# Kernel optimization log

Measured on AMD Instinct MI355X. Metric: run time of the kernel, lower is better.

Reference implementation:

```python
import jax, jax.numpy as jnp
import numpy as np

N_EMBED = 384
NUM_HEADS = 6
HEAD_SIZE = 64
B, T = 128, 256


def setup_inputs() -> dict:
    key = jax.random.key(0)
    ks = jax.random.split(key, 6)
    x = jax.random.normal(ks[0], (B, T, N_EMBED), dtype=jnp.float32)
    s = 0.02
    Wq = jax.random.normal(ks[1], (NUM_HEADS, N_EMBED, HEAD_SIZE), dtype=jnp.float32) * s
    Wk = jax.random.normal(ks[2], (NUM_HEADS, N_EMBED, HEAD_SIZE), dtype=jnp.float32) * s
    Wv = jax.random.normal(ks[3], (NUM_HEADS, N_EMBED, HEAD_SIZE), dtype=jnp.float32) * s
    Wp = jax.random.normal(ks[4], (NUM_HEADS * HEAD_SIZE, N_EMBED), dtype=jnp.float32) * s
    bp = jnp.zeros((N_EMBED,), dtype=jnp.float32)
    return {"x": x, "Wq": Wq, "Wk": Wk, "Wv": Wv, "Wp": Wp, "bp": bp}


def reference(x, Wq, Wk, Wv, Wp, bp):
    # x: [B,T,C]; Wq/Wk/Wv: [H,C,hs]; Wp: [H*hs, C]
    Bx, Tx, C = x.shape
    q = jnp.einsum('btc,hcd->bhtd', x, Wq)
    k = jnp.einsum('btc,hcd->bhtd', x, Wk)
    v = jnp.einsum('btc,hcd->bhtd', x, Wv)
    scale = HEAD_SIZE ** (-0.5)
    scores = jnp.einsum('bhtd,bhsd->bhts', q, k) * scale  # [B,H,T,T]
    causal = jnp.tril(jnp.ones((Tx, Tx), dtype=bool))
    scores = jnp.where(causal, scores, -jnp.inf)
    attn = jax.nn.softmax(scores, axis=-1)
    # dropout is identity in eval mode
    out = jnp.einsum('bhts,bhsd->bhtd', attn, v)  # [B,H,T,hs]
    out = out.transpose(0, 2, 1, 3).reshape(Bx, Tx, NUM_HEADS * HEAD_SIZE)
    return out @ Wp + bp
```

## Files before the change

### kernel.cpp

```cpp
#include <hip/hip_runtime.h>
#include <hip/hip_bf16.h>

#define C_DIM 384
#define H_NUM 6
#define HS    64
#define B_DIM 128
#define T_DIM 256
#define NROWS (B_DIM * T_DIM)

typedef unsigned short u16;
typedef unsigned int u32;
typedef short bf16x8 __attribute__((ext_vector_type(8)));
typedef float floatx4 __attribute__((ext_vector_type(4)));

__device__ __forceinline__ u16 f2b(float f) {
  __hip_bfloat16 h = __float2bfloat16(f);
  u16 u;
  __builtin_memcpy(&u, &h, 2);
  return u;
}
__device__ __forceinline__ void gload_lds16(const void* g, void* lds) {
  __builtin_amdgcn_global_load_lds(
      (const __attribute__((address_space(1))) u32*)g,
      (__attribute__((address_space(3))) u32*)lds, 16, 0, 0);
}

__global__ __launch_bounds__(256) void prep_kernel(
    const float* __restrict__ x, const float* __restrict__ Wq,
    const float* __restrict__ Wk, const float* __restrict__ Wv,
    const float* __restrict__ Wp, u16* __restrict__ xb,
    u16* __restrict__ Wh, u16* __restrict__ Wpt) {
  const int bid = blockIdx.x;
  const int tid = threadIdx.x;
  if (bid < 6144) {
    const int i = bid * 256 + tid;
    const float4 f0 = ((const float4*)x)[i * 2];
    const float4 f1 = ((const float4*)x)[i * 2 + 1];
    bf16x8 pk;
    pk[0] = (short)f2b(f0.x); pk[1] = (short)f2b(f0.y);
    pk[2] = (short)f2b(f0.z); pk[3] = (short)f2b(f0.w);
    pk[4] = (short)f2b(f1.x); pk[5] = (short)f2b(f1.y);
    pk[6] = (short)f2b(f1.z); pk[7] = (short)f2b(f1.w);
    ((bf16x8*)xb)[i] = pk;
  } else {
    const int idx = (bid - 6144) * 256 + tid;
    const int WHN = H_NUM * 192 * C_DIM;
    if (idx < WHN) {
      int h = idx / (192 * C_DIM);
      int rem = idx % (192 * C_DIM);
      int r = rem / C_DIM, c = rem % C_DIM;
      int tz = r >> 6, d = r & 63;
      const float* W = (tz == 0) ? Wq : (tz == 1) ? Wk : Wv;
      Wh[idx] = f2b(W[((size_t)h * C_DIM + c) * HS + d]);
    } else {
      int j = idx - WHN;
      int n = j / C_DIM, c = j % C_DIM;
      Wpt[j] = f2b(Wp[c * C_DIM + n]);
    }
  }
}

__global__ __launch_bounds__(256) void qkv_gemm(
    const u16* __restrict__ xb, const u16* __restrict__ Wh,
    u16* __restrict__ q, u16* __restrict__ k, u16* __restrict__ vT) {
  __shared__ u16 smem[20480];
  u16* As = smem;
  u16* Bs = smem + 8192;
  u16* Ts = smem;
  const int row0 = blockIdx.x * 128;
  const int h = blockIdx.y;
  const u16* a_rows = xb + (size_t)row0 * C_DIM;
  const u16* wbase = Wh + (size_t)h * 192 * C_DIM;

  const int tid = threadIdx.x;
  const int lane = tid & 63;
  const int w = tid >> 6;
  const int lr = lane >> 3;
  const int lkc = (lane & 7) * 8;
  const int qd = lane >> 4;
  const int ln = lane & 15;
  const int wm = (w & 1) * 64;
  const int wn = (w >> 1) * 96;

  floatx4 acc[4][6];
#pragma unroll
  for (int i = 0; i < 4; ++i)
#pragma unroll
    for (int j = 0; j < 6; ++j) acc[i][j] = floatx4{0.f, 0.f, 0.f, 0.f};

  for (int kb = 0; kb < C_DIM / 64; ++kb) {
    const int k0 = kb * 64;
    __syncthreads();
#pragma unroll
    for (int s = 0; s < 4; ++s) {
      const int rbase = (s * 4 + w) * 8;
      gload_lds16(a_rows + (size_t)(rbase + lr) * C_DIM + k0 + lkc,
                  As + rbase * 64);
    }
#pragma unroll
    for (int s = 0; s < 6; ++s) {
      const int rbase = (s * 4 + w) * 8;
      gload_lds16(wbase + (size_t)(rbase + lr) * C_DIM + k0 + lkc,
                  Bs + rbase * 64);
    }
    __syncthreads();

#pragma unroll
    for (int kk = 0; kk < 2; ++kk) {
      bf16x8 af[4], bf[6];
#pragma unroll
      for (int mt = 0; mt < 4; ++mt)
        af[mt] = *(const bf16x8*)&As[(wm + mt * 16 + ln) * 64 + kk * 32 + qd * 8];
#pragma unroll
      for (int nt = 0; nt < 6; ++nt)
        bf[nt] = *(const bf16x8*)&Bs[(wn + nt * 16 + ln) * 64 + kk * 32 + qd * 8];
#pragma unroll
      for (int mt = 0; mt < 4; ++mt)
#pragma unroll
        for (int nt = 0; nt < 6; ++nt)
          acc[mt][nt] = __builtin_amdgcn_mfma_f32_16x16x32_bf16(
              af[mt], bf[nt], acc[mt][nt], 0, 0, 0);
    }
  }

  const int b = row0 >> 8;
  const int t0 = row0 & 255;
  __syncthreads();

#pragma unroll
  for (int nt = 0; nt < 6; ++nt) {
    const int c0 = wn + nt * 16;
    const int tz = c0 >> 6;
    const int d = (c0 & 63) + ln;
#pragma unroll
    for (int mt = 0; mt < 4; ++mt) {
#pragma unroll
      for (int r = 0; r < 4; ++r) {
        const int tl = wm + mt * 16 + qd * 4 + r;
        const u16 val = f2b(acc[mt][nt][r]);
        if (tz == 0)
          q[(((size_t)b * H_NUM + h) * T_DIM + t0 + tl) * HS + d] = val;
        else if (tz == 1)
          k[(((size_t)b * H_NUM + h) * T_DIM + t0 + tl) * HS + d] = val;
        else
          Ts[d * 136 + tl] = val;
      }
    }
  }
  __syncthreads();
#pragma unroll
  for (int it = 0; it < 4; ++it) {
    const int idx = it * 256 + tid;
    const int d_l = idx >> 4, tc = idx & 15;
    *(uint4*)&vT[(((size_t)b * H_NUM + h) * HS + d_l) * T_DIM + t0 + tc * 8] =
        *(const uint4*)&Ts[d_l * 136 + tc * 8];
  }
}

template <bool DIAG>
__device__ __forceinline__ void attn_chunk(int c, int mt, int lane, int ln,
                                           int qd, const bf16x8* qf,
                                           const u16* Kls, u16* Pw,
                                           const u16* vTg, floatx4* oacc,
                                           float* lsum) {
  floatx4 sacc[4];
#pragma unroll
  for (int st = 0; st < 4; ++st) {
    sacc[st] = floatx4{0.f, 0.f, 0.f, 0.f};
#pragma unroll
    for (int kc = 0; kc < 2; ++kc) {
      bf16x8 kf = *(const bf16x8*)&Kls[((c * 4 + st) * 2 + kc) * 512 + lane * 8];
      sacc[st] =
          __builtin_amdgcn_mfma_f32_16x16x32_bf16(qf[kc], kf, sacc[st], 0, 0, 0);
    }
  }
#pragma unroll
  for (int st = 0; st < 4; ++st) {
#pragma unroll
    for (int r = 0; r < 4; ++r) {
      const float sv = sacc[st][r] * 0.125f;
      float p = __expf(sv);
      if (DIAG) {
        const bool ok = (c * 64 + st * 16 + ln) <= (mt * 16 + qd * 4 + r);
        p = ok ? p : 0.f;
      }
      lsum[r] += p;
      Pw[(qd * 4 + r) * 72 + st * 16 + ln] = f2b(p);
    }
  }
#pragma unroll
  for (int kc2 = 0; kc2 < 2; ++kc2) {
    bf16x8 pf = *(const bf16x8*)&Pw[ln * 72 + kc2 * 32 + qd * 8];
#pragma unroll
    for (int dt = 0; dt < 4; ++dt) {
      bf16x8 vf = *(const bf16x8*)(vTg + (dt * 16 + ln) * 256 + c * 64 +
                                   kc2 * 32 + qd * 8);
      oacc[dt] =
          __builtin_amdgcn_mfma_f32_16x16x32_bf16(pf, vf, oacc[dt], 0, 0, 0);
    }
  }
}

__global__ __launch_bounds__(256) void attn_mfma(
    const u16* __restrict__ q, const u16* __restrict__ k,
    const u16* __restrict__ vT, u16* __restrict__ y) {
  __shared__ u16 Kls[32 * 512];
  __shared__ u16 Pls[4 * 1152];
  const int bh = blockIdx.x;
  const int b = bh / H_NUM, h = bh % H_NUM;
  const int tid = threadIdx.x, lane = tid & 63, w = tid >> 6;
  const int ln = lane & 15, qd = lane >> 4;
  const u16* qg = q + (size_t)bh * (T_DIM * HS);
  const u16* kg = k + (size_t)bh * (T_DIM * HS);
  const u16* vTg = vT + (size_t)bh * (HS * T_DIM);
  u16* Pw = Pls + w * 1152;

#pragma unroll
  for (int ff = 0; ff < 8; ++ff) {
    const int fid = w * 8 + ff;
    const int S16 = fid >> 1, kc = fid & 1;
    gload_lds16(kg + (S16 * 16 + ln) * 64 + kc * 32 + qd * 8, &Kls[fid * 512]);
  }
  __syncthreads();

#pragma unroll
  for (int i = 0; i < 4; ++i) {
    const int mt = i * 4 + w;
    bf16x8 qf[2];
#pragma unroll
    for (int kc = 0; kc < 2; ++kc)
      qf[kc] = *(const bf16x8*)(qg + (mt * 16 + ln) * 64 + kc * 32 + qd * 8);

    floatx4 oacc[4];
    float lsum[4];
#pragma unroll
    for (int dt = 0; dt < 4; ++dt) oacc[dt] = floatx4{0.f, 0.f, 0.f, 0.f};
#pragma unroll
    for (int r = 0; r < 4; ++r) lsum[r] = 0.f;

    const int cmax = mt >> 2;
    for (int c = 0; c < cmax; ++c)
      attn_chunk<false>(c, mt, lane, ln, qd, qf, Kls, Pw, vTg, oacc, lsum);
    attn_chunk<true>(cmax, mt, lane, ln, qd, qf, Kls, Pw, vTg, oacc, lsum);

#pragma unroll
    for (int off = 1; off < 16; off <<= 1)
#pragma unroll
      for (int r = 0; r < 4; ++r) lsum[r] += __shfl_xor(lsum[r], off);

#pragma unroll
    for (int r = 0; r < 4; ++r) {
      const float inv = 1.f / lsum[r];
      const int t = mt * 16 + qd * 4 + r;
      u16* yo = y + ((size_t)b * T_DIM + t) * C_DIM + h * HS;
#pragma unroll
      for (int dt = 0; dt < 4; ++dt) yo[dt * 16 + ln] = f2b(oacc[dt][r] * inv);
    }
  }
}

__global__ __launch_bounds__(256) void proj_gemm(
    const u16* __restrict__ yb, const u16* __restrict__ Wpt,
    const float* __restrict__ bp, float* __restrict__ out) {
  __shared__ u16 As[128 * 64];
  __shared__ u16 Bs[128 * 64];
  const int row0 = blockIdx.x * 128;
  const int n0 = blockIdx.y * 128;
  const u16* a_rows = yb + (size_t)row0 * C_DIM;
  const u16* bt_rows = Wpt + (size_t)n0 * C_DIM;

  const int tid = threadIdx.x;
  const int lane = tid & 63;
  const int w = tid >> 6;
  const int lr = lane >> 3;
  const int lkc = (lane & 7) * 8;
  const int qd = lane >> 4;
  const int ln = lane & 15;
  const int mw = (w >> 1) * 64;
  const int nw = (w & 1) * 64;

  floatx4 acc[4][4];
#pragma unroll
  for (int i = 0; i < 4; ++i)
#pragma unroll
    for (int j = 0; j < 4; ++j) acc[i][j] = floatx4{0.f, 0.f, 0.f, 0.f};

  for (int kb = 0; kb < C_DIM / 64; ++kb) {
    const int k0 = kb * 64;
    __syncthreads();
#pragma unroll
    for (int s = 0; s < 4; ++s) {
      const int rbase = (s * 4 + w) * 8;
      gload_lds16(a_rows + (size_t)(rbase + lr) * C_DIM + k0 + lkc,
                  As + rbase * 64);
      gload_lds16(bt_rows + (size_t)(rbase + lr) * C_DIM + k0 + lkc,
                  Bs + rbase * 64);
    }
    __syncthreads();

#pragma unroll
    for (int kk = 0; kk < 2; ++kk) {
      bf16x8 af[4], bf[4];
#pragma unroll
      for (int mt = 0; mt < 4; ++mt)
        af[mt] = *(const bf16x8*)&As[(mw + mt * 16 + ln) * 64 + kk * 32 + qd * 8];
#pragma unroll
      for (int nt = 0; nt < 4; ++nt)
        bf[nt] = *(const bf16x8*)&Bs[(nw + nt * 16 + ln) * 64 + kk * 32 + qd * 8];
#pragma unroll
      for (int mt = 0; mt < 4; ++mt)
#pragma unroll
        for (int nt = 0; nt < 4; ++nt)
          acc[mt][nt] = __builtin_amdgcn_mfma_f32_16x16x32_bf16(
              af[mt], bf[nt], acc[mt][nt], 0, 0, 0);
    }
  }

#pragma unroll
  for (int nt = 0; nt < 4; ++nt) {
    const int col = n0 + nw + nt * 16 + ln;
    const float bias = bp[col];
#pragma unroll
    for (int mt = 0; mt < 4; ++mt) {
#pragma unroll
      for (int r = 0; r < 4; ++r) {
        const int grow = row0 + mw + mt * 16 + qd * 4 + r;
        out[(size_t)grow * C_DIM + col] = acc[mt][nt][r] + bias;
      }
    }
  }
}

extern "C" void kernel_launch(void* const* d_in, const int* in_sizes, int n_in,
                              void* d_out, int out_size, void* d_ws, size_t ws_size,
                              hipStream_t stream) {
  const float* x  = (const float*)d_in[0];
  const float* Wq = (const float*)d_in[1];
  const float* Wk = (const float*)d_in[2];
  const float* Wv = (const float*)d_in[3];
  const float* Wp = (const float*)d_in[4];
  const float* bp = (const float*)d_in[5];
  float* out = (float*)d_out;

  const size_t n_x = (size_t)NROWS * C_DIM;
  const size_t qkv_elems = (size_t)B_DIM * H_NUM * T_DIM * HS;

  u16* Wh  = (u16*)d_ws;
  u16* Wpt = Wh + (size_t)H_NUM * 192 * C_DIM;
  u16* xb  = Wpt + C_DIM * C_DIM;
  u16* q   = xb + n_x;
  u16* k   = q + qkv_elems;
  u16* vT  = k + qkv_elems;
  u16* y   = xb;

  prep_kernel<<<6144 + 2304, 256, 0, stream>>>(x, Wq, Wk, Wv, Wp, xb, Wh, Wpt);
  qkv_gemm<<<dim3(NROWS / 128, H_NUM), 256, 0, stream>>>(xb, Wh, q, k, vT);
  attn_mfma<<<B_DIM * H_NUM, 256, 0, stream>>>(q, k, vT, y);
  proj_gemm<<<dim3(NROWS / 128, 3), 256, 0, stream>>>(y, Wpt, bp, out);
}
```

Before: 224.4 us.

## Fuse QKV projection and causal attention into one kernel using shared memory

Merges the QKV GEMM and the attention kernel into a single 512-thread block per (batch, head). Q, K and V^T now stay in LDS instead of round-tripping through global memory. V^T is stored with an XOR swizzle to avoid bank conflicts. The causal work is balanced by pairing query tiles w and 15-w per wave. The cost is a large LDS footprint (~114KB) that limits occupancy, and the number of blocks drops to 768.

```diff
diff --git a/kernel.cpp b/kernel.cpp
--- a/kernel.cpp
+++ b/kernel.cpp
@@ -60,116 +60,24 @@
   }
 }
 
-__global__ __launch_bounds__(256) void qkv_gemm(
-    const u16* __restrict__ xb, const u16* __restrict__ Wh,
-    u16* __restrict__ q, u16* __restrict__ k, u16* __restrict__ vT) {
-  __shared__ u16 smem[20480];
-  u16* As = smem;
-  u16* Bs = smem + 8192;
-  u16* Ts = smem;
-  const int row0 = blockIdx.x * 128;
-  const int h = blockIdx.y;
-  const u16* a_rows = xb + (size_t)row0 * C_DIM;
-  const u16* wbase = Wh + (size_t)h * 192 * C_DIM;
-
-  const int tid = threadIdx.x;
-  const int lane = tid & 63;
-  const int w = tid >> 6;
-  const int lr = lane >> 3;
-  const int lkc = (lane & 7) * 8;
-  const int qd = lane >> 4;
-  const int ln = lane & 15;
-  const int wm = (w & 1) * 64;
-  const int wn = (w >> 1) * 96;
-
-  floatx4 acc[4][6];
-#pragma unroll
-  for (int i = 0; i < 4; ++i)
-#pragma unroll
-    for (int j = 0; j < 6; ++j) acc[i][j] = floatx4{0.f, 0.f, 0.f, 0.f};
-
-  for (int kb = 0; kb < C_DIM / 64; ++kb) {
-    const int k0 = kb * 64;
-    __syncthreads();
-#pragma unroll
-    for (int s = 0; s < 4; ++s) {
-      const int rbase = (s * 4 + w) * 8;
-      gload_lds16(a_rows + (size_t)(rbase + lr) * C_DIM + k0 + lkc,
-                  As + rbase * 64);
-    }
-#pragma unroll
-    for (int s = 0; s < 6; ++s) {
-      const int rbase = (s * 4 + w) * 8;
-      gload_lds16(wbase + (size_t)(rbase + lr) * C_DIM + k0 + lkc,
-                  Bs + rbase * 64);
-    }
-    __syncthreads();
-
-#pragma unroll
-    for (int kk = 0; kk < 2; ++kk) {
-      bf16x8 af[4], bf[6];
-#pragma unroll
-      for (int mt = 0; mt < 4; ++mt)
-        af[mt] = *(const bf16x8*)&As[(wm + mt * 16 + ln) * 64 + kk * 32 + qd * 8];
-#pragma unroll
-      for (int nt = 0; nt < 6; ++nt)
-        bf[nt] = *(const bf16x8*)&Bs[(wn + nt * 16 + ln) * 64 + kk * 32 + qd * 8];
-#pragma unroll
-      for (int mt = 0; mt < 4; ++mt)
-#pragma unroll
-        for (int nt = 0; nt < 6; ++nt)
-          acc[mt][nt] = __builtin_amdgcn_mfma_f32_16x16x32_bf16(
-              af[mt], bf[nt], acc[mt][nt], 0, 0, 0);
-    }
-  }
-
-  const int b = row0 >> 8;
-  const int t0 = row0 & 255;
-  __syncthreads();
-
-#pragma unroll
-  for (int nt = 0; nt < 6; ++nt) {
-    const int c0 = wn + nt * 16;
-    const int tz = c0 >> 6;
-    const int d = (c0 & 63) + ln;
-#pragma unroll
-    for (int mt = 0; mt < 4; ++mt) {
-#pragma unroll
-      for (int r = 0; r < 4; ++r) {
-        const int tl = wm + mt * 16 + qd * 4 + r;
-        const u16 val = f2b(acc[mt][nt][r]);
-        if (tz == 0)
-          q[(((size_t)b * H_NUM + h) * T_DIM + t0 + tl) * HS + d] = val;
-        else if (tz == 1)
-          k[(((size_t)b * H_NUM + h) * T_DIM + t0 + tl) * HS + d] = val;
-        else
-          Ts[d * 136 + tl] = val;
-      }
-    }
-  }
-  __syncthreads();
-#pragma unroll
-  for (int it = 0; it < 4; ++it) {
-    const int idx = it * 256 + tid;
-    const int d_l = idx >> 4, tc = idx & 15;
-    *(uint4*)&vT[(((size_t)b * H_NUM + h) * HS + d_l) * T_DIM + t0 + tc * 8] =
-        *(const uint4*)&Ts[d_l * 136 + tc * 8];
-  }
-}
+#define QS_OFF  0
+#define KLS_OFF 16384
+#define VTS_OFF 32768
+#define PLS_OFF 49152
 
 template <bool DIAG>
-__device__ __forceinline__ void attn_chunk(int c, int mt, int lane, int ln,
-                                           int qd, const bf16x8* qf,
-                                           const u16* Kls, u16* Pw,
-                                           const u16* vTg, floatx4* oacc,
-                                           float* lsum) {
+__device__ __forceinline__ void attn_chunk_f(int c, int mt, int lane, int ln,
+                                             int qd, const bf16x8* qf,
+                                             const u16* smem, u16* Pw,
+                                             floatx4* oacc, float* lsum) {
   floatx4 sacc[4];
 #pragma unroll
   for (int st = 0; st < 4; ++st) {
     sacc[st] = floatx4{0.f, 0.f, 0.f, 0.f};
 #pragma unroll
     for (int kc = 0; kc < 2; ++kc) {
-      bf16x8 kf = *(const bf16x8*)&Kls[((c * 4 + st) * 2 + kc) * 512 + lane * 8];
+      bf16x8 kf = *(const bf16x8*)&smem[KLS_OFF + ((c * 4 + st) * 2 + kc) * 512 +
+                                        lane * 8];
       sacc[st] =
           __builtin_amdgcn_mfma_f32_16x16x32_bf16(qf[kc], kf, sacc[st], 0, 0, 0);
     }
@@ -193,43 +101,111 @@
     bf16x8 pf = *(const bf16x8*)&Pw[ln * 72 + kc2 * 32 + qd * 8];
 #pragma unroll
     for (int dt = 0; dt < 4; ++dt) {
-      bf16x8 vf = *(const bf16x8*)(vTg + (dt * 16 + ln) * 256 + c * 64 +
-                                   kc2 * 32 + qd * 8);
+      bf16x8 vf = *(const bf16x8*)&smem[VTS_OFF + (dt * 16 + ln) * 256 +
+                                        ((c * 64 + kc2 * 32 + qd * 8) ^
+                                         ((ln & 7) << 3))];
       oacc[dt] =
           __builtin_amdgcn_mfma_f32_16x16x32_bf16(pf, vf, oacc[dt], 0, 0, 0);
     }
   }
 }
 
-__global__ __launch_bounds__(256) void attn_mfma(
-    const u16* __restrict__ q, const u16* __restrict__ k,
-    const u16* __restrict__ vT, u16* __restrict__ y) {
-  __shared__ u16 Kls[32 * 512];
-  __shared__ u16 Pls[4 * 1152];
-  const int bh = blockIdx.x;
-  const int b = bh / H_NUM, h = bh % H_NUM;
-  const int tid = threadIdx.x, lane = tid & 63, w = tid >> 6;
-  const int ln = lane & 15, qd = lane >> 4;
-  const u16* qg = q + (size_t)bh * (T_DIM * HS);
-  const u16* kg = k + (size_t)bh * (T_DIM * HS);
-  const u16* vTg = vT + (size_t)bh * (HS * T_DIM);
-  u16* Pw = Pls + w * 1152;
-
-#pragma unroll
-  for (int ff = 0; ff < 8; ++ff) {
-    const int fid = w * 8 + ff;
-    const int S16 = fid >> 1, kc = fid & 1;
-    gload_lds16(kg + (S16 * 16 + ln) * 64 + kc * 32 + qd * 8, &Kls[fid * 512]);
+__global__ __launch_bounds__(512) void qkv_attn_fused(
+    const u16* __restrict__ xb, const u16* __restrict__ Wh,
+    u16* __restrict__ y) {
+  __shared__ __align__(16) u16 smem[58368];
+  const int b = blockIdx.x;
+  const int h = blockIdx.y;
+  const u16* a_rows = xb + (size_t)b * 256 * C_DIM;
+  const u16* wbase = Wh + (size_t)h * 192 * C_DIM;
+
+  const int tid = threadIdx.x;
+  const int lane = tid & 63;
+  const int w = tid >> 6;
+  const int lr = lane >> 3;
+  const int lkc = (lane & 7) * 8;
+  const int qd = lane >> 4;
+  const int ln = lane & 15;
+  const int wm = (w >> 1) * 64;
+  const int wn = (w & 1) * 96;
+
+  floatx4 acc[4][6];
+#pragma unroll
+  for (int i = 0; i < 4; ++i)
+#pragma unroll
+    for (int j = 0; j < 6; ++j) acc[i][j] = floatx4{0.f, 0.f, 0.f, 0.f};
+
+  for (int kb = 0; kb < C_DIM / 64; ++kb) {
+    const int k0 = kb * 64;
+    __syncthreads();
+#pragma unroll
+    for (int s = 0; s < 4; ++s) {
+      const int rbase = (s * 8 + w) * 8;
+      gload_lds16(a_rows + (size_t)(rbase + lr) * C_DIM + k0 + lkc,
+                  smem + rbase * 64);
+    }
+#pragma unroll
+    for (int s = 0; s < 3; ++s) {
+      const int rbase = (s * 8 + w) * 8;
+      gload_lds16(wbase + (size_t)(rbase + lr) * C_DIM + k0 + lkc,
+                  smem + KLS_OFF + rbase * 64);
+    }
+    __syncthreads();
+
+#pragma unroll
+    for (int kk = 0; kk < 2; ++kk) {
+      bf16x8 af[4], bf[6];
+#pragma unroll
+      for (int mt = 0; mt < 4; ++mt)
+        af[mt] =
+            *(const bf16x8*)&smem[(wm + mt * 16 + ln) * 64 + kk * 32 + qd * 8];
+#pragma unroll
+      for (int nt = 0; nt < 6; ++nt)
+        bf[nt] = *(const bf16x8*)&smem[KLS_OFF + (wn + nt * 16 + ln) * 64 +
+                                       kk * 32 + qd * 8];
+#pragma unroll
+      for (int mt = 0; mt < 4; ++mt)
+#pragma unroll
+        for (int nt = 0; nt < 6; ++nt)
+          acc[mt][nt] = __builtin_amdgcn_mfma_f32_16x16x32_bf16(
+              af[mt], bf[nt], acc[mt][nt], 0, 0, 0);
+    }
   }
   __syncthreads();
 
 #pragma unroll
-  for (int i = 0; i < 4; ++i) {
-    const int mt = i * 4 + w;
+  for (int nt = 0; nt < 6; ++nt) {
+    const int c0 = wn + nt * 16;
+#pragma unroll
+    for (int mt = 0; mt < 4; ++mt) {
+#pragma unroll
+      for (int r = 0; r < 4; ++r) {
+        const int t = wm + mt * 16 + qd * 4 + r;
+        const u16 val = f2b(acc[mt][nt][r]);
+        if (c0 < 64) {
+          smem[QS_OFF + t * 64 + c0 + ln] = val;
+        } else if (c0 < 128) {
+          const int d = c0 - 64 + ln;
+          smem[KLS_OFF + ((t >> 4) << 10) + ((d >> 5) << 9) +
+               (((d >> 3) & 3) << 7) + ((t & 15) << 3) + (d & 7)] = val;
+        } else {
+          const int dv = c0 - 128 + ln;
+          smem[VTS_OFF + dv * 256 + (t ^ ((dv & 7) << 3))] = val;
+        }
+      }
+    }
+  }
+  __syncthreads();
+
+  u16* Pw = smem + PLS_OFF + w * 1152;
+#pragma unroll
+  for (int i = 0; i < 2; ++i) {
+    const int mt = i ? (15 - w) : w;
     bf16x8 qf[2];
 #pragma unroll
     for (int kc = 0; kc < 2; ++kc)
-      qf[kc] = *(const bf16x8*)(qg + (mt * 16 + ln) * 64 + kc * 32 + qd * 8);
+      qf[kc] = *(const bf16x8*)&smem[QS_OFF + (mt * 16 + ln) * 64 + kc * 32 +
+                                     qd * 8];
 
     floatx4 oacc[4];
     float lsum[4];
@@ -240,8 +216,8 @@
 
     const int cmax = mt >> 2;
     for (int c = 0; c < cmax; ++c)
-      attn_chunk<false>(c, mt, lane, ln, qd, qf, Kls, Pw, vTg, oacc, lsum);
-    attn_chunk<true>(cmax, mt, lane, ln, qd, qf, Kls, Pw, vTg, oacc, lsum);
+      attn_chunk_f<false>(c, mt, lane, ln, qd, qf, smem, Pw, oacc, lsum);
+    attn_chunk_f<true>(cmax, mt, lane, ln, qd, qf, smem, Pw, oacc, lsum);
 
 #pragma unroll
     for (int off = 1; off < 16; off <<= 1)
@@ -343,18 +319,13 @@
   float* out = (float*)d_out;
 
   const size_t n_x = (size_t)NROWS * C_DIM;
-  const size_t qkv_elems = (size_t)B_DIM * H_NUM * T_DIM * HS;
 
   u16* Wh  = (u16*)d_ws;
   u16* Wpt = Wh + (size_t)H_NUM * 192 * C_DIM;
   u16* xb  = Wpt + C_DIM * C_DIM;
-  u16* q   = xb + n_x;
-  u16* k   = q + qkv_elems;
-  u16* vT  = k + qkv_elems;
-  u16* y   = xb;
+  u16* y   = xb + n_x;
 
   prep_kernel<<<6144 + 2304, 256, 0, stream>>>(x, Wq, Wk, Wv, Wp, xb, Wh, Wpt);
-  qkv_gemm<<<dim3(NROWS / 128, H_NUM), 256, 0, stream>>>(xb, Wh, q, k, vT);
-  attn_mfma<<<B_DIM * H_NUM, 256, 0, stream>>>(q, k, vT, y);
+  qkv_attn_fused<<<dim3(B_DIM, H_NUM), 512, 0, stream>>>(xb, Wh, y);
   proj_gemm<<<dim3(NROWS / 128, 3), 256, 0, stream>>>(y, Wpt, bp, out);
 }
```

Measured after the change: 199.8 us. -10.9%, faster.
